# Kernel optimization log

Hardware: AMD Instinct MI355X
Metric: run time of the kernel (lower is better)

The kernel has to match this reference:

```python
import jax, jax.numpy as jnp
import numpy as np


def setup_inputs() -> dict:
    key = jax.random.key(0)
    k1, k2, k3 = jax.random.split(key, 3)
    B, N, K = 512, 1024, 64  # batch, seq_len, num_tags
    y_pred = jax.random.normal(k1, (B, N, K), dtype=jnp.float32)
    # glorot-uniform-ish init for the transition matrix
    limit = np.sqrt(6.0 / (K + K)).astype(np.float32)
    trans = jax.random.uniform(k2, (K, K), dtype=jnp.float32, minval=-limit, maxval=limit)
    y_true = jax.random.randint(k3, (B, N), 0, K, dtype=jnp.int32)
    return {"y_pred": y_pred, "trans": trans, "y_true": y_true}


def _crf_loss(y_pred, trans, y_true):
    # mask derived from padding convention: padded frames have logits <= -1e6
    mask = jnp.all(y_pred > -1e6, axis=2, keepdims=True).astype(y_pred.dtype)  # [B,N,1]
    y_pred = y_pred * mask
    m = mask[..., 0]  # [B,N]

    # ---- target (gold-path) score ----
    # point score: emission logits at the gold labels (one-hot einsum == gather)
    point = jnp.sum(
        jnp.take_along_axis(y_pred, y_true[..., None], axis=2)[..., 0] * m, axis=1
    )  # [B]
    # transition score: trans[y_t, y_{t+1}], zeroed where either frame is masked
    tvals = trans[y_true[:, :-1], y_true[:, 1:]] * m[:, :-1] * m[:, 1:]  # [B,N-1]
    target_score = point + jnp.sum(tvals, axis=1)  # [B]

    # ---- log normalizer via forward recursion (logsumexp semiring scan) ----
    init = y_pred[:, 0]  # [B,K]
    emits = jnp.swapaxes(y_pred[:, 1:], 0, 1)  # [N-1,B,K]
    masks = jnp.swapaxes(mask[:, 1:], 0, 1)    # [N-1,B,1]

    def step(alpha, xm):
        emit, mm = xm
        # alpha: [B,K] -> broadcast over next-tag axis with trans [K,K]
        new = jax.nn.logsumexp(alpha[:, :, None] + trans[None], axis=1) + emit
        alpha = mm * new + (1.0 - mm) * alpha
        return alpha, None

    alpha, _ = jax.lax.scan(step, init, (emits, masks))
    log_norm = jax.nn.logsumexp(alpha, axis=1)  # [B]
    return log_norm - target_score


def reference(y_pred, trans, y_true):
    return _crf_loss(y_pred, trans, y_true)
```

## Files before the change

### kernel.cpp

```cpp
#include <hip/hip_runtime.h>
#include <cstdint>
#include <cstddef>


constexpr int Nn = 1024;
constexpr int Kk = 64;
constexpr float LOG2E = 1.4426950408889634f;
constexpr float LN2   = 0.6931471805599453f;

typedef float f32x4  __attribute__((ext_vector_type(4)));
typedef short short8 __attribute__((ext_vector_type(8)));
typedef int   int32x4 __attribute__((ext_vector_type(4)));

__device__ __forceinline__ float fast_exp2(float x) {
#if __has_builtin(__builtin_amdgcn_exp2f)
    return __builtin_amdgcn_exp2f(x);
#else
    return exp2f(x);
#endif
}

__device__ __forceinline__ int cvt_pk_bf16(float lo, float hi) {
    int r;
    asm("v_cvt_pk_bf16_f32 %0, %1, %2" : "=v"(r) : "v"(lo), "v"(hi));
    return r;
}

__device__ __forceinline__ short bf16_rne(float x) {
    unsigned u = __builtin_bit_cast(unsigned, x);
    unsigned r = u + 0x7FFFu + ((u >> 16) & 1u);
    return (short)(r >> 16);
}

__device__ __forceinline__ short8 load_afrag(const float* __restrict__ trans,
                                             int n, int blk, int mt, int kt) {
    short8 r;
#pragma unroll
    for (int q = 0; q < 8; ++q) {
        int k = kt * 32 + (q >> 2) * 16 + 4 * blk + (q & 3);
        float v = fast_exp2(trans[k * Kk + mt * 16 + n] * LOG2E);
        r[q] = bf16_rne(v);
    }
    return r;
}

__device__ __forceinline__ int clamp_s(int s) {
    return s < -100 ? -100 : (s > 100 ? 100 : s);
}

__device__ __forceinline__ void stage4(const float* src, float* dstbase) {
#pragma unroll
    for (int mt = 0; mt < 4; ++mt) {
        __builtin_amdgcn_global_load_lds(
            (const __attribute__((address_space(1))) unsigned*)(src + mt * 16),
            (__attribute__((address_space(3))) unsigned*)(dstbase + mt * 256),
            16, 0, 0);
    }
}

#define MFMA16(a, b, c) __builtin_amdgcn_mfma_f32_16x16x32_bf16((a), (b), (c), 0, 0, 0)

__global__ __launch_bounds__(64, 1) void crf_fwd(
    const float* __restrict__ y_pred,
    const float* __restrict__ trans,
    float* __restrict__ out)
{
    const int l   = threadIdx.x;
    const int n   = l & 15;
    const int blk = l >> 4;

    __shared__ __align__(16) float lds[8 * 1024];

    const float* yp  = y_pred + (size_t)(blockIdx.x * 16 + n) * (Nn * Kk);
    const float* ypn = yp + 4 * blk;

    short8 a00 = load_afrag(trans, n, blk, 0, 0), a01 = load_afrag(trans, n, blk, 0, 1);
    short8 a10 = load_afrag(trans, n, blk, 1, 0), a11 = load_afrag(trans, n, blk, 1, 1);
    short8 a20 = load_afrag(trans, n, blk, 2, 0), a21 = load_afrag(trans, n, blk, 2, 1);
    short8 a30 = load_afrag(trans, n, blk, 3, 0), a31 = load_afrag(trans, n, blk, 3, 1);

    f32x4 c0, c1, c2, c3;
    {
        f32x4 e0 = *(const f32x4*)(ypn);
        f32x4 e1 = *(const f32x4*)(ypn + 16);
        f32x4 e2 = *(const f32x4*)(ypn + 32);
        f32x4 e3 = *(const f32x4*)(ypn + 48);
        float M0_ = yp[0];
        c0.x = fast_exp2((e0.x - M0_) * LOG2E); c0.y = fast_exp2((e0.y - M0_) * LOG2E);
        c0.z = fast_exp2((e0.z - M0_) * LOG2E); c0.w = fast_exp2((e0.w - M0_) * LOG2E);
        c1.x = fast_exp2((e1.x - M0_) * LOG2E); c1.y = fast_exp2((e1.y - M0_) * LOG2E);
        c1.z = fast_exp2((e1.z - M0_) * LOG2E); c1.w = fast_exp2((e1.w - M0_) * LOG2E);
        c2.x = fast_exp2((e2.x - M0_) * LOG2E); c2.y = fast_exp2((e2.y - M0_) * LOG2E);
        c2.z = fast_exp2((e2.z - M0_) * LOG2E); c2.w = fast_exp2((e2.w - M0_) * LOG2E);
        c3.x = fast_exp2((e3.x - M0_) * LOG2E); c3.y = fast_exp2((e3.y - M0_) * LOG2E);
        c3.z = fast_exp2((e3.z - M0_) * LOG2E); c3.w = fast_exp2((e3.w - M0_) * LOG2E);
    }
    const float M0 = yp[0];

    short8 b0, b1;
    {
        int p0 = cvt_pk_bf16(c0.x, c0.y), p1 = cvt_pk_bf16(c0.z, c0.w);
        int p2 = cvt_pk_bf16(c1.x, c1.y), p3 = cvt_pk_bf16(c1.z, c1.w);
        int p4 = cvt_pk_bf16(c2.x, c2.y), p5 = cvt_pk_bf16(c2.z, c2.w);
        int p6 = cvt_pk_bf16(c3.x, c3.y), p7 = cvt_pk_bf16(c3.z, c3.w);
        b0 = __builtin_bit_cast(short8, (int32x4){p0, p1, p2, p3});
        b1 = __builtin_bit_cast(short8, (int32x4){p4, p5, p6, p7});
    }

    int s_use;
    {
        float v = __shfl(c0.x, n);
        s_use = clamp_s((int)((__builtin_bit_cast(unsigned, v) >> 23) & 0xFFu) - 127);
    }
    int Sacc = 0;

#pragma unroll
    for (int t = 1; t <= 8; ++t) {
        stage4(ypn + t * 64, &lds[(t & 7) * 1024]);
    }

    const float CLO = 1e-30f, CHI = 1e30f;

#define PE_APPLY(CN, EM) \
    c##CN.x = fminf(fmaxf(d##CN.x * fast_exp2(fmaf(EM.x, LOG2E, msu_)), CLO), CHI); \
    c##CN.y = fminf(fmaxf(d##CN.y * fast_exp2(fmaf(EM.y, LOG2E, msu_)), CLO), CHI); \
    c##CN.z = fminf(fmaxf(d##CN.z * fast_exp2(fmaf(EM.z, LOG2E, msu_)), CLO), CHI); \
    c##CN.w = fminf(fmaxf(d##CN.w * fast_exp2(fmaf(EM.w, LOG2E, msu_)), CLO), CHI);

#pragma unroll 4
    for (int t = 1; t < Nn; ++t) {
        f32x4 z4_ = {0.f, 0.f, 0.f, 0.f};
        f32x4 d0 = MFMA16(a00, b0, MFMA16(a01, b1, z4_));
        f32x4 d1 = MFMA16(a10, b0, MFMA16(a11, b1, z4_));
        f32x4 d2 = MFMA16(a20, b0, MFMA16(a21, b1, z4_));
        f32x4 d3 = MFMA16(a30, b0, MFMA16(a31, b1, z4_));

        asm volatile("s_waitcnt vmcnt(28)" ::: "memory");

        const float* emb = &lds[(t & 7) * 1024] + l * 4;
        f32x4 em0 = *(const f32x4*)(emb);
        f32x4 em1 = *(const f32x4*)(emb + 256);
        f32x4 em2 = *(const f32x4*)(emb + 512);
        f32x4 em3 = *(const f32x4*)(emb + 768);

        int ts = t + 8 > Nn - 1 ? Nn - 1 : t + 8;
        stage4(ypn + ts * 64, &lds[(t & 7) * 1024]);

        float msu_ = -(float)s_use;
        Sacc += s_use;
        PE_APPLY(0, em0) PE_APPLY(1, em1)
        PE_APPLY(2, em2) PE_APPLY(3, em3)

        float bc_ = __shfl(c0.x, n);
        s_use = clamp_s((int)((__builtin_bit_cast(unsigned, bc_) >> 23) & 0xFFu) - 127);

        int p0_ = cvt_pk_bf16(c0.x, c0.y), p1_ = cvt_pk_bf16(c0.z, c0.w);
        int p2_ = cvt_pk_bf16(c1.x, c1.y), p3_ = cvt_pk_bf16(c1.z, c1.w);
        int p4_ = cvt_pk_bf16(c2.x, c2.y), p5_ = cvt_pk_bf16(c2.z, c2.w);
        int p6_ = cvt_pk_bf16(c3.x, c3.y), p7_ = cvt_pk_bf16(c3.z, c3.w);
        b0 = __builtin_bit_cast(short8, (int32x4){p0_, p1_, p2_, p3_});
        b1 = __builtin_bit_cast(short8, (int32x4){p4_, p5_, p6_, p7_});
    }

    asm volatile("s_waitcnt vmcnt(0)" ::: "memory");

    float sum = ((c0.x + c0.y) + (c0.z + c0.w)) + ((c1.x + c1.y) + (c1.z + c1.w))
              + ((c2.x + c2.y) + (c2.z + c2.w)) + ((c3.x + c3.y) + (c3.z + c3.w));
    sum += __shfl_xor(sum, 16);
    sum += __shfl_xor(sum, 32);
    float log_norm = (log2f(sum) + (float)Sacc) * LN2 + M0;
    if (l < 16) {
        out[blockIdx.x * 16 + l] += log_norm;
    }
}

__global__ __launch_bounds__(64) void crf_target(
    const float* __restrict__ y_pred,
    const float* __restrict__ trans,
    const int*   __restrict__ y_true,
    float* __restrict__ out)
{
    const int b = blockIdx.x, l = threadIdx.x;
    const int* ytb = y_true + (size_t)b * Nn;
    const float* ypb = y_pred + (size_t)b * Nn * Kk;
    float v = 0.0f;
#pragma unroll
    for (int i = 0; i < 16; ++i) {
        int t = i * 64 + l;
        int y0 = ytb[t];
        v += ypb[(size_t)t * Kk + y0];
        if (t < Nn - 1) {
            int y1 = ytb[t + 1];
            v += trans[y0 * Kk + y1];
        }
    }
#pragma unroll
    for (int off = 32; off; off >>= 1) v += __shfl_xor(v, off);
    if (l == 0) out[b] = -v;
}

extern "C" void kernel_launch(void* const* d_in, const int* in_sizes, int n_in,
                              void* d_out, int out_size, void* d_ws, size_t ws_size,
                              hipStream_t stream) {
    const float* y_pred = (const float*)d_in[0];
    const float* trans  = (const float*)d_in[1];
    const int*   y_true = (const int*)d_in[2];
    float* out = (float*)d_out;

    crf_target<<<512, 64, 0, stream>>>(y_pred, trans, y_true, out);
    crf_fwd<<<32, 64, 0, stream>>>(y_pred, trans, out);
}
```

Measured before the change: 341.5 us.

## Switch CRF forward MFMA to fp16, prefetch next-step emissions, trim clamping

Replaces the bf16 MFMA and manual bf16 rounding with fp16 MFMA fed through packed round-toward-zero conversions. The recursion loop is rewritten as a manually two-way unrolled macro that loads the next step's emissions from LDS one iteration ahead, overlapping LDS latency with the MFMA chain. The per-element clamp drops the lower bound and caps at 60000 to stay within fp16 range. Precision changes: fp16 has more mantissa bits but a narrow exponent range, so values that underflow now flush to zero instead of being held at a floor.

```diff
diff --git a/kernel.cpp b/kernel.cpp
--- a/kernel.cpp
+++ b/kernel.cpp
@@ -9,7 +9,7 @@
 constexpr float LN2   = 0.6931471805599453f;
 
 typedef float f32x4  __attribute__((ext_vector_type(4)));
-typedef short short8 __attribute__((ext_vector_type(8)));
+typedef _Float16 half8 __attribute__((ext_vector_type(8)));
 typedef int   int32x4 __attribute__((ext_vector_type(4)));
 
 __device__ __forceinline__ float fast_exp2(float x) {
@@ -20,26 +20,18 @@
 #endif
 }
 
-__device__ __forceinline__ int cvt_pk_bf16(float lo, float hi) {
-    int r;
-    asm("v_cvt_pk_bf16_f32 %0, %1, %2" : "=v"(r) : "v"(lo), "v"(hi));
-    return r;
-}
-
-__device__ __forceinline__ short bf16_rne(float x) {
-    unsigned u = __builtin_bit_cast(unsigned, x);
-    unsigned r = u + 0x7FFFu + ((u >> 16) & 1u);
-    return (short)(r >> 16);
-}
-
-__device__ __forceinline__ short8 load_afrag(const float* __restrict__ trans,
-                                             int n, int blk, int mt, int kt) {
-    short8 r;
+__device__ __forceinline__ int pkrtz(float lo, float hi) {
+    return __builtin_bit_cast(int, __builtin_amdgcn_cvt_pkrtz(lo, hi));
+}
+
+__device__ __forceinline__ half8 load_afrag(const float* __restrict__ trans,
+                                            int n, int blk, int mt, int kt) {
+    half8 r;
 #pragma unroll
     for (int q = 0; q < 8; ++q) {
         int k = kt * 32 + (q >> 2) * 16 + 4 * blk + (q & 3);
         float v = fast_exp2(trans[k * Kk + mt * 16 + n] * LOG2E);
-        r[q] = bf16_rne(v);
+        r[q] = (_Float16)v;
     }
     return r;
 }
@@ -58,7 +50,7 @@
     }
 }
 
-#define MFMA16(a, b, c) __builtin_amdgcn_mfma_f32_16x16x32_bf16((a), (b), (c), 0, 0, 0)
+#define MFMA16(a, b, c) __builtin_amdgcn_mfma_f32_16x16x32_f16((a), (b), (c), 0, 0, 0)
 
 __global__ __launch_bounds__(64, 1) void crf_fwd(
     const float* __restrict__ y_pred,
@@ -74,10 +66,10 @@
     const float* yp  = y_pred + (size_t)(blockIdx.x * 16 + n) * (Nn * Kk);
     const float* ypn = yp + 4 * blk;
 
-    short8 a00 = load_afrag(trans, n, blk, 0, 0), a01 = load_afrag(trans, n, blk, 0, 1);
-    short8 a10 = load_afrag(trans, n, blk, 1, 0), a11 = load_afrag(trans, n, blk, 1, 1);
-    short8 a20 = load_afrag(trans, n, blk, 2, 0), a21 = load_afrag(trans, n, blk, 2, 1);
-    short8 a30 = load_afrag(trans, n, blk, 3, 0), a31 = load_afrag(trans, n, blk, 3, 1);
+    half8 a00 = load_afrag(trans, n, blk, 0, 0), a01 = load_afrag(trans, n, blk, 0, 1);
+    half8 a10 = load_afrag(trans, n, blk, 1, 0), a11 = load_afrag(trans, n, blk, 1, 1);
+    half8 a20 = load_afrag(trans, n, blk, 2, 0), a21 = load_afrag(trans, n, blk, 2, 1);
+    half8 a30 = load_afrag(trans, n, blk, 3, 0), a31 = load_afrag(trans, n, blk, 3, 1);
 
     f32x4 c0, c1, c2, c3;
     {
@@ -97,15 +89,10 @@
     }
     const float M0 = yp[0];
 
-    short8 b0, b1;
-    {
-        int p0 = cvt_pk_bf16(c0.x, c0.y), p1 = cvt_pk_bf16(c0.z, c0.w);
-        int p2 = cvt_pk_bf16(c1.x, c1.y), p3 = cvt_pk_bf16(c1.z, c1.w);
-        int p4 = cvt_pk_bf16(c2.x, c2.y), p5 = cvt_pk_bf16(c2.z, c2.w);
-        int p6 = cvt_pk_bf16(c3.x, c3.y), p7 = cvt_pk_bf16(c3.z, c3.w);
-        b0 = __builtin_bit_cast(short8, (int32x4){p0, p1, p2, p3});
-        b1 = __builtin_bit_cast(short8, (int32x4){p4, p5, p6, p7});
-    }
+    half8 b0 = __builtin_bit_cast(half8, (int32x4){pkrtz(c0.x, c0.y), pkrtz(c0.z, c0.w),
+                                                   pkrtz(c1.x, c1.y), pkrtz(c1.z, c1.w)});
+    half8 b1 = __builtin_bit_cast(half8, (int32x4){pkrtz(c2.x, c2.y), pkrtz(c2.z, c2.w),
+                                                   pkrtz(c3.x, c3.y), pkrtz(c3.z, c3.w)});
 
     int s_use;
     {
@@ -114,53 +101,60 @@
     }
     int Sacc = 0;
 
+    asm volatile("s_waitcnt vmcnt(0)" ::: "memory");
+
 #pragma unroll
     for (int t = 1; t <= 8; ++t) {
         stage4(ypn + t * 64, &lds[(t & 7) * 1024]);
     }
 
-    const float CLO = 1e-30f, CHI = 1e30f;
-
-#define PE_APPLY(CN, EM) \
-    c##CN.x = fminf(fmaxf(d##CN.x * fast_exp2(fmaf(EM.x, LOG2E, msu_)), CLO), CHI); \
-    c##CN.y = fminf(fmaxf(d##CN.y * fast_exp2(fmaf(EM.y, LOG2E, msu_)), CLO), CHI); \
-    c##CN.z = fminf(fmaxf(d##CN.z * fast_exp2(fmaf(EM.z, LOG2E, msu_)), CLO), CHI); \
-    c##CN.w = fminf(fmaxf(d##CN.w * fast_exp2(fmaf(EM.w, LOG2E, msu_)), CLO), CHI);
-
-#pragma unroll 4
-    for (int t = 1; t < Nn; ++t) {
-        f32x4 z4_ = {0.f, 0.f, 0.f, 0.f};
-        f32x4 d0 = MFMA16(a00, b0, MFMA16(a01, b1, z4_));
-        f32x4 d1 = MFMA16(a10, b0, MFMA16(a11, b1, z4_));
-        f32x4 d2 = MFMA16(a20, b0, MFMA16(a21, b1, z4_));
-        f32x4 d3 = MFMA16(a30, b0, MFMA16(a31, b1, z4_));
-
-        asm volatile("s_waitcnt vmcnt(28)" ::: "memory");
-
-        const float* emb = &lds[(t & 7) * 1024] + l * 4;
-        f32x4 em0 = *(const f32x4*)(emb);
-        f32x4 em1 = *(const f32x4*)(emb + 256);
-        f32x4 em2 = *(const f32x4*)(emb + 512);
-        f32x4 em3 = *(const f32x4*)(emb + 768);
-
-        int ts = t + 8 > Nn - 1 ? Nn - 1 : t + 8;
-        stage4(ypn + ts * 64, &lds[(t & 7) * 1024]);
-
-        float msu_ = -(float)s_use;
-        Sacc += s_use;
-        PE_APPLY(0, em0) PE_APPLY(1, em1)
-        PE_APPLY(2, em2) PE_APPLY(3, em3)
-
-        float bc_ = __shfl(c0.x, n);
-        s_use = clamp_s((int)((__builtin_bit_cast(unsigned, bc_) >> 23) & 0xFFu) - 127);
-
-        int p0_ = cvt_pk_bf16(c0.x, c0.y), p1_ = cvt_pk_bf16(c0.z, c0.w);
-        int p2_ = cvt_pk_bf16(c1.x, c1.y), p3_ = cvt_pk_bf16(c1.z, c1.w);
-        int p4_ = cvt_pk_bf16(c2.x, c2.y), p5_ = cvt_pk_bf16(c2.z, c2.w);
-        int p6_ = cvt_pk_bf16(c3.x, c3.y), p7_ = cvt_pk_bf16(c3.z, c3.w);
-        b0 = __builtin_bit_cast(short8, (int32x4){p0_, p1_, p2_, p3_});
-        b1 = __builtin_bit_cast(short8, (int32x4){p4_, p5_, p6_, p7_});
-    }
+    asm volatile("s_waitcnt vmcnt(28)" ::: "memory");
+    f32x4 emc0, emc1, emc2, emc3, emn0, emn1, emn2, emn3;
+    {
+        const float* eb = &lds[1 * 1024] + l * 4;
+        emc0 = *(const f32x4*)(eb);       emc1 = *(const f32x4*)(eb + 256);
+        emc2 = *(const f32x4*)(eb + 512); emc3 = *(const f32x4*)(eb + 768);
+    }
+
+    const float CHI = 60000.0f;
+
+#define PE1(CN, EM) \
+    c##CN.x = fminf(d##CN.x * fast_exp2(fmaf(EM.x, LOG2E, msu_)), CHI); \
+    c##CN.y = fminf(d##CN.y * fast_exp2(fmaf(EM.y, LOG2E, msu_)), CHI); \
+    c##CN.z = fminf(d##CN.z * fast_exp2(fmaf(EM.z, LOG2E, msu_)), CHI); \
+    c##CN.w = fminf(d##CN.w * fast_exp2(fmaf(EM.w, LOG2E, msu_)), CHI);
+
+#define STEP(T, EI0, EI1, EI2, EI3, EO0, EO1, EO2, EO3) { \
+    f32x4 zz_ = {0.f, 0.f, 0.f, 0.f}; \
+    f32x4 d0 = MFMA16(a00, b0, MFMA16(a01, b1, zz_)); \
+    f32x4 d1 = MFMA16(a10, b0, MFMA16(a11, b1, zz_)); \
+    f32x4 d2 = MFMA16(a20, b0, MFMA16(a21, b1, zz_)); \
+    f32x4 d3 = MFMA16(a30, b0, MFMA16(a31, b1, zz_)); \
+    asm volatile("s_waitcnt vmcnt(24)" ::: "memory"); \
+    { const float* nb_ = &lds[(((T) + 1) & 7) * 1024] + l * 4; \
+      EO0 = *(const f32x4*)(nb_);       EO1 = *(const f32x4*)(nb_ + 256); \
+      EO2 = *(const f32x4*)(nb_ + 512); EO3 = *(const f32x4*)(nb_ + 768); } \
+    float msu_ = -(float)s_use; \
+    Sacc += s_use; \
+    PE1(0, EI0) \
+    float bc_ = __shfl(c0.x, n); \
+    PE1(1, EI1) PE1(2, EI2) PE1(3, EI3) \
+    s_use = clamp_s((int)((__builtin_bit_cast(unsigned, bc_) >> 23) & 0xFFu) - 127); \
+    asm volatile("" ::: "memory"); \
+    { int ts_ = (T) + 8 > Nn - 1 ? Nn - 1 : (T) + 8; \
+      stage4(ypn + ts_ * 64, &lds[((T) & 7) * 1024]); } \
+    b0 = __builtin_bit_cast(half8, (int32x4){pkrtz(c0.x, c0.y), pkrtz(c0.z, c0.w), \
+                                             pkrtz(c1.x, c1.y), pkrtz(c1.z, c1.w)}); \
+    b1 = __builtin_bit_cast(half8, (int32x4){pkrtz(c2.x, c2.y), pkrtz(c2.z, c2.w), \
+                                             pkrtz(c3.x, c3.y), pkrtz(c3.z, c3.w)}); \
+}
+
+    for (int tb = 0; tb < 511; ++tb) {
+        const int t = 2 * tb + 1;
+        STEP(t,     emc0, emc1, emc2, emc3, emn0, emn1, emn2, emn3)
+        STEP(t + 1, emn0, emn1, emn2, emn3, emc0, emc1, emc2, emc3)
+    }
+    STEP(1023, emc0, emc1, emc2, emc3, emn0, emn1, emn2, emn3)
 
     asm volatile("s_waitcnt vmcnt(0)" ::: "memory");
 
```

After: 327.3 us. 1.04x faster.
